# Kernel tuning notes

Measured on AMD Instinct MI355X. Metric: run time of the kernel, lower is better.

## Reference

```python
import jax, jax.numpy as jnp
import numpy as np

B, S, D = 8, 2048, 1024

def setup_inputs() -> dict:
    key = jax.random.key(0)
    ks = jax.random.split(key, 7)
    s = 1.0 / np.sqrt(D)
    return {
        "x": jax.random.normal(ks[0], (B, S, D), dtype=jnp.float32),
        "Wq": jax.random.normal(ks[1], (D, D), dtype=jnp.float32) * s,
        "bq": jnp.zeros((D,), dtype=jnp.float32),
        "Wk": jax.random.normal(ks[2], (D, D), dtype=jnp.float32) * s,
        "bk": jnp.zeros((D,), dtype=jnp.float32),
        "Wv": jax.random.normal(ks[3], (D, D), dtype=jnp.float32) * s,
        "bv": jnp.zeros((D,), dtype=jnp.float32),
    }

def reference(x, Wq, bq, Wk, bk, Wv, bv):
    # QKV projections: [B,S,D]
    q = x @ Wq + bq
    k = x @ Wk + bk
    v = x @ Wv + bv
    # scores scaled by sqrt(full input_dim) — single head, per source
    scores = jnp.einsum("bsd,btd->bst", q, k) / jnp.sqrt(jnp.float32(D))
    attn = jax.nn.softmax(scores, axis=2)
    return jnp.einsum("bst,btd->bsd", attn, v)
```

## Files before the change

### kernel.cpp

```cpp
#include <hip/hip_runtime.h>

typedef _Float16 half8 __attribute__((ext_vector_type(8)));
typedef float floatx4 __attribute__((ext_vector_type(4)));

#define AS1 __attribute__((address_space(1)))
#define AS3 __attribute__((address_space(3)))

__global__ __launch_bounds__(256) void wtrans_kernel(
    const float* __restrict__ W0, const float* __restrict__ W1,
    const float* __restrict__ W2, _Float16* __restrict__ Wt)
{
    __shared__ _Float16 t[64 * 72];
    const float* W = (blockIdx.z == 0) ? W0 : (blockIdx.z == 1) ? W1 : W2;
    _Float16* O = Wt + (long)blockIdx.z * 1048576;
    const int tid = threadIdx.x;
    const int kb = blockIdx.y * 64, nb = blockIdx.x * 64;
#pragma unroll
    for (int i = 0; i < 4; i++) {
        int r = (tid >> 4) + i * 16;
        int c = (tid & 15) * 4;
        floatx4 w = *(const floatx4*)&W[(long)(kb + r) * 1024 + nb + c];
#pragma unroll
        for (int j = 0; j < 4; j++) t[(c + j) * 72 + r] = (_Float16)w[j];
    }
    __syncthreads();
    const int c = tid >> 2, rch = (tid & 3) * 16;
    half8 v0 = *(const half8*)&t[c * 72 + rch];
    half8 v1 = *(const half8*)&t[c * 72 + rch + 8];
    _Float16* o = &O[(long)(nb + c) * 1024 + kb + rch];
    *(half8*)o = v0;
    *(half8*)(o + 8) = v1;
}

__global__ __launch_bounds__(256) void f32_to_f16_kernel(
    const float* __restrict__ in, _Float16* __restrict__ out, int n)
{
    for (long i = ((long)blockIdx.x * 256 + threadIdx.x) * 8; i < n;
         i += (long)gridDim.x * 256 * 8) {
        floatx4 a = *(const floatx4*)&in[i];
        floatx4 b = *(const floatx4*)&in[i + 4];
        half8 h;
#pragma unroll
        for (int e = 0; e < 4; e++) { h[e] = (_Float16)a[e]; h[e + 4] = (_Float16)b[e]; }
        *(half8*)&out[i] = h;
    }
}

template <int MODE>
__global__ __launch_bounds__(256) void gemm128_kernel(
    const _Float16* __restrict__ A, const _Float16* __restrict__ Bt,
    void* __restrict__ Cv, const float* __restrict__ bias,
    const float* __restrict__ bias2, float* __restrict__ R,
    int nx, int ny,
    int K, int lda, int ldb, int ldc,
    long aBatch, long bBatch, long cBatch, float scale)
{
    constexpr int SMEM_ELEMS = (MODE == 1) ? 17408 : 16384;
    __shared__ _Float16 smem[SMEM_ELEMS];
    _Float16* Ash = smem;
    _Float16* Bsh = smem + 8192;

    const int tid = threadIdx.x;
    const int wave = tid >> 6, lane = tid & 63;
    const int quad = lane >> 4, lr = lane & 15;
    const int wm = wave & 1, wn = wave >> 1;

    const int P = gridDim.x >> 3;
    const int g = (blockIdx.x & 7) * P + (blockIdx.x >> 3);
    const int pplane = nx * ny;
    const int z = g / pplane;
    const int rr = g - z * pplane;
    const int by = rr / nx;
    const int bx = rr - by * nx;
    const int m0 = by * 128, n0 = bx * 128;

    const _Float16* Ab = A + (long)z * aBatch;
    const _Float16* Bb = Bt + (long)z * bBatch;

    const int srow = tid >> 2;
    const int scol = ((tid & 3) ^ ((srow >> 1) & 3)) * 8;
    const long ag0 = (long)(m0 + srow) * lda + scol;
    const long bg0 = (long)(n0 + srow) * ldb + scol;
    const int sdst = tid * 8;

    floatx4 acc[4][4] = {};

    for (int k0 = 0; k0 < K; k0 += 64) {
#pragma unroll
        for (int s = 0; s < 2; s++) {
            const int kk = k0 + s * 32;
            const int so = s * 4096;
            __builtin_amdgcn_global_load_lds(
                (AS1 void*)(Ab + ag0 + kk), (AS3 void*)(Ash + so + sdst), 16, 0, 0);
            __builtin_amdgcn_global_load_lds(
                (AS1 void*)(Ab + ag0 + (long)64 * lda + kk), (AS3 void*)(Ash + so + sdst + 2048), 16, 0, 0);
            __builtin_amdgcn_global_load_lds(
                (AS1 void*)(Bb + bg0 + kk), (AS3 void*)(Bsh + so + sdst), 16, 0, 0);
            __builtin_amdgcn_global_load_lds(
                (AS1 void*)(Bb + bg0 + (long)64 * ldb + kk), (AS3 void*)(Bsh + so + sdst + 2048), 16, 0, 0);
        }
        __syncthreads();

        const int slotA = (quad ^ ((lr >> 1) & 3)) * 8;
#pragma unroll
        for (int s = 0; s < 2; s++) {
            const int so = s * 4096;
            half8 aF[4], bF[4];
#pragma unroll
            for (int i = 0; i < 4; i++) {
                aF[i] = *(const half8*)&Ash[so + (wm * 64 + i * 16 + lr) * 32 + slotA];
                bF[i] = *(const half8*)&Bsh[so + (wn * 64 + i * 16 + lr) * 32 + slotA];
            }
#pragma unroll
            for (int mi = 0; mi < 4; mi++)
#pragma unroll
                for (int ni = 0; ni < 4; ni++)
                    acc[mi][ni] = __builtin_amdgcn_mfma_f32_16x16x32_f16(
                        aF[mi], bF[ni], acc[mi][ni], 0, 0, 0);
        }
        __syncthreads();
    }

    if constexpr (MODE == 0) {
        _Float16* C = (_Float16*)Cv + (long)z * cBatch;
        const float* bz = (z == 0 || !bias2) ? bias : bias2;
#pragma unroll
        for (int ni = 0; ni < 4; ni++) {
            const int n = n0 + wn * 64 + ni * 16 + lr;
            const float bv_ = bz ? bz[n] : 0.0f;
#pragma unroll
            for (int mi = 0; mi < 4; mi++) {
                const int mb = m0 + wm * 64 + mi * 16 + quad * 4;
#pragma unroll
                for (int r = 0; r < 4; r++)
                    C[(long)(mb + r) * ldc + n] = (_Float16)(acc[mi][ni][r] + bv_);
            }
        }
    } else if constexpr (MODE == 1) {
        _Float16* ctile = smem;
#pragma unroll
        for (int ni = 0; ni < 4; ni++) {
            const int nl = wn * 64 + ni * 16 + lr;
            const float bv_ = bias ? bias[n0 + nl] : 0.0f;
#pragma unroll
            for (int mi = 0; mi < 4; mi++) {
                const int ml = wm * 64 + mi * 16 + quad * 4;
#pragma unroll
                for (int r = 0; r < 4; r++)
                    ctile[nl * 136 + ml + r] = (_Float16)(acc[mi][ni][r] + bv_);
            }
        }
        __syncthreads();
        _Float16* C = (_Float16*)Cv + (long)(m0 >> 11) * cBatch;
        const int t0 = m0 & 2047;
#pragma unroll
        for (int p = 0; p < 8; p++) {
            const int row = p * 16 + (tid >> 4);
            const int seg = (tid & 15) * 8;
            half8 v = *(const half8*)&ctile[row * 136 + seg];
            *(half8*)&C[(long)(n0 + row) * ldc + t0 + seg] = v;
        }
    } else if constexpr (MODE == 2) {
        float* C = (float*)Cv + (long)z * cBatch;
        const float* Rz = R + (long)z * 2048;
        float inv[4][4];
#pragma unroll
        for (int mi = 0; mi < 4; mi++) {
            const int mb = m0 + wm * 64 + mi * 16 + quad * 4;
#pragma unroll
            for (int r = 0; r < 4; r++) inv[mi][r] = 1.0f / Rz[mb + r];
        }
#pragma unroll
        for (int ni = 0; ni < 4; ni++) {
            const int n = n0 + wn * 64 + ni * 16 + lr;
#pragma unroll
            for (int mi = 0; mi < 4; mi++) {
                const int mb = m0 + wm * 64 + mi * 16 + quad * 4;
#pragma unroll
                for (int r = 0; r < 4; r++)
                    C[(long)(mb + r) * ldc + n] = acc[mi][ni][r] * inv[mi][r];
            }
        }
    } else {
        _Float16* C = (_Float16*)Cv + (long)z * cBatch;
        float* Rz = R + (long)z * 2048;
        float rs[4][4] = {};
#pragma unroll
        for (int ni = 0; ni < 4; ni++) {
            const int n = n0 + wn * 64 + ni * 16 + lr;
#pragma unroll
            for (int mi = 0; mi < 4; mi++) {
                const int mb = m0 + wm * 64 + mi * 16 + quad * 4;
#pragma unroll
                for (int r = 0; r < 4; r++) {
                    float e = __expf(acc[mi][ni][r] * scale);
                    C[(long)(mb + r) * ldc + n] = (_Float16)e;
                    rs[mi][r] += e;
                }
            }
        }
#pragma unroll
        for (int off = 1; off < 16; off <<= 1)
#pragma unroll
            for (int mi = 0; mi < 4; mi++)
#pragma unroll
                for (int r = 0; r < 4; r++)
                    rs[mi][r] += __shfl_xor(rs[mi][r], off, 64);
        if (lr == 0) {
#pragma unroll
            for (int mi = 0; mi < 4; mi++) {
                const int mb = m0 + wm * 64 + mi * 16 + quad * 4;
#pragma unroll
                for (int r = 0; r < 4; r++)
                    atomicAdd(&Rz[mb + r], rs[mi][r]);
            }
        }
    }
}

extern "C" void kernel_launch(void* const* d_in, const int* in_sizes, int n_in,
                              void* d_out, int out_size, void* d_ws, size_t ws_size,
                              hipStream_t stream)
{
    const float* x  = (const float*)d_in[0];
    const float* Wq = (const float*)d_in[1];
    const float* bq = (const float*)d_in[2];
    const float* Wk = (const float*)d_in[3];
    const float* bk = (const float*)d_in[4];
    const float* Wv = (const float*)d_in[5];
    const float* bv = (const float*)d_in[6];

    if (ws_size < 174129152u) return;

    char* ws = (char*)d_ws;
    _Float16* Q  = (_Float16*)(ws + 0);
    _Float16* Vt = (_Float16*)(ws + 67108864);
    _Float16* Sc = (_Float16*)(ws + 100663296);
    _Float16* Wt = (_Float16*)(ws + 167772160);
    float*    R  = (float*)(ws + 174063616);
    _Float16* xb = Sc;
    _Float16* Kb = Q + 16777216;
    float* out = (float*)d_out;

    hipMemsetAsync(R, 0, 65536, stream);
    wtrans_kernel<<<dim3(16, 16, 3), 256, 0, stream>>>(Wq, Wk, Wv, Wt);
    f32_to_f16_kernel<<<2048, 256, 0, stream>>>(x, xb, 16777216);

    gemm128_kernel<0><<<2048, 256, 0, stream>>>(
        xb, Wt, Q, bq, bk, nullptr, 8, 128, 1024, 1024, 1024, 1024,
        0, 1048576, 16777216, 1.0f);
    gemm128_kernel<1><<<1024, 256, 0, stream>>>(
        xb, Wt + 2097152, Vt, bv, nullptr, nullptr, 8, 128, 1024, 1024, 1024, 2048,
        0, 0, 2097152, 1.0f);

    gemm128_kernel<3><<<2048, 256, 0, stream>>>(
        Q, Kb, Sc, nullptr, nullptr, R, 16, 16, 1024, 1024, 1024, 2048,
        2097152, 2097152, 4194304, 0.03125f);

    gemm128_kernel<2><<<1024, 256, 0, stream>>>(
        Sc, Vt, out, nullptr, nullptr, R, 8, 16, 2048, 2048, 2048, 1024,
        4194304, 2097152, 2097152, 1.0f);
}
```

Before: 480.5 us.

## Add producer warp with triple-buffered LDS ring for GEMM loads

Each GEMM block gains a fifth wave that acts as a dedicated producer. It issues global-to-LDS loads into a three-stage ring buffer and signals the four consumer waves through shared-memory ready/done counters, replacing the two block-wide barriers per K step. The aim is to overlap memory loads with MFMA compute. It adds spin-waiting, more LDS per block (about 48KB, which may reduce occupancy) and a subtle synchronisation protocol. The softmax row-sum atomics are also reworked so each lane issues one atomic instead of lane 0 issuing sixteen.

```diff
diff --git a/kernel.cpp b/kernel.cpp
--- a/kernel.cpp
+++ b/kernel.cpp
@@ -5,6 +5,8 @@
 
 #define AS1 __attribute__((address_space(1)))
 #define AS3 __attribute__((address_space(3)))
+
+#define WAIT_VMCNT(n) __builtin_amdgcn_s_waitcnt(((n) & 15) | (((n) >> 4) << 14) | (7 << 4) | (15 << 8))
 
 __global__ __launch_bounds__(256) void wtrans_kernel(
     const float* __restrict__ W0, const float* __restrict__ W1,
@@ -47,7 +49,7 @@
 }
 
 template <int MODE>
-__global__ __launch_bounds__(256) void gemm128_kernel(
+__global__ __launch_bounds__(320) void gemm128_kernel(
     const _Float16* __restrict__ A, const _Float16* __restrict__ Bt,
     void* __restrict__ Cv, const float* __restrict__ bias,
     const float* __restrict__ bias2, float* __restrict__ R,
@@ -55,15 +57,13 @@
     int K, int lda, int ldb, int ldc,
     long aBatch, long bBatch, long cBatch, float scale)
 {
-    constexpr int SMEM_ELEMS = (MODE == 1) ? 17408 : 16384;
-    __shared__ _Float16 smem[SMEM_ELEMS];
-    _Float16* Ash = smem;
-    _Float16* Bsh = smem + 8192;
+    __shared__ _Float16 ring[3 * 8192];
+    __shared__ int ready;
+    __shared__ int done;
 
     const int tid = threadIdx.x;
-    const int wave = tid >> 6, lane = tid & 63;
-    const int quad = lane >> 4, lr = lane & 15;
-    const int wm = wave & 1, wn = wave >> 1;
+    if (tid == 0) { ready = 0; done = 0; }
+    __syncthreads();
 
     const int P = gridDim.x >> 3;
     const int g = (blockIdx.x & 7) * P + (blockIdx.x >> 3);
@@ -76,49 +76,81 @@
 
     const _Float16* Ab = A + (long)z * aBatch;
     const _Float16* Bb = Bt + (long)z * bBatch;
-
-    const int srow = tid >> 2;
-    const int scol = ((tid & 3) ^ ((srow >> 1) & 3)) * 8;
-    const long ag0 = (long)(m0 + srow) * lda + scol;
-    const long bg0 = (long)(n0 + srow) * ldb + scol;
-    const int sdst = tid * 8;
+    const int S = K >> 5;
+
+    if (tid >= 256) {
+        const int pl = tid - 256;
+        const int prow = pl >> 2;
+        const int pcol = (((pl & 3) ^ ((prow >> 1) & 3))) * 8;
+        const _Float16* aB = Ab + (long)(m0 + prow) * lda + pcol;
+        const _Float16* bB = Bb + (long)(n0 + prow) * ldb + pcol;
+
+        auto issue = [&](int s) {
+            _Float16* dst = ring + (s % 3) * 8192 + pl * 8;
+            const _Float16* a = aB + s * 32;
+            const _Float16* b = bB + s * 32;
+#pragma unroll
+            for (int i = 0; i < 8; i++)
+                __builtin_amdgcn_global_load_lds(
+                    (AS1 void*)(a + (long)i * 16 * lda), (AS3 void*)(dst + i * 512), 16, 0, 0);
+#pragma unroll
+            for (int i = 0; i < 8; i++)
+                __builtin_amdgcn_global_load_lds(
+                    (AS1 void*)(b + (long)i * 16 * ldb), (AS3 void*)(dst + 4096 + i * 512), 16, 0, 0);
+        };
+
+        issue(0);
+        issue(1);
+        int dn = 0;
+        for (int s = 0; s + 2 < S; s++) {
+            if (s >= 1 && dn < 4 * s) {
+                do {
+                    dn = __hip_atomic_load(&done, __ATOMIC_ACQUIRE, __HIP_MEMORY_SCOPE_WORKGROUP);
+                    if (dn < 4 * s) __builtin_amdgcn_s_sleep(1);
+                } while (dn < 4 * s);
+            }
+            issue(s + 2);
+            WAIT_VMCNT(32);
+            __hip_atomic_store(&ready, s + 1, __ATOMIC_RELEASE, __HIP_MEMORY_SCOPE_WORKGROUP);
+        }
+        WAIT_VMCNT(16);
+        __hip_atomic_store(&ready, S - 1, __ATOMIC_RELEASE, __HIP_MEMORY_SCOPE_WORKGROUP);
+        WAIT_VMCNT(0);
+        __hip_atomic_store(&ready, S, __ATOMIC_RELEASE, __HIP_MEMORY_SCOPE_WORKGROUP);
+        if constexpr (MODE == 1) { __syncthreads(); __syncthreads(); }
+        return;
+    }
+
+    const int wave = tid >> 6, lane = tid & 63;
+    const int quad = lane >> 4, lr = lane & 15;
+    const int wm = wave & 1, wn = wave >> 1;
+    const int slotA = (quad ^ ((lr >> 1) & 3)) * 8;
 
     floatx4 acc[4][4] = {};
-
-    for (int k0 = 0; k0 < K; k0 += 64) {
-#pragma unroll
-        for (int s = 0; s < 2; s++) {
-            const int kk = k0 + s * 32;
-            const int so = s * 4096;
-            __builtin_amdgcn_global_load_lds(
-                (AS1 void*)(Ab + ag0 + kk), (AS3 void*)(Ash + so + sdst), 16, 0, 0);
-            __builtin_amdgcn_global_load_lds(
-                (AS1 void*)(Ab + ag0 + (long)64 * lda + kk), (AS3 void*)(Ash + so + sdst + 2048), 16, 0, 0);
-            __builtin_amdgcn_global_load_lds(
-                (AS1 void*)(Bb + bg0 + kk), (AS3 void*)(Bsh + so + sdst), 16, 0, 0);
-            __builtin_amdgcn_global_load_lds(
-                (AS1 void*)(Bb + bg0 + (long)64 * ldb + kk), (AS3 void*)(Bsh + so + sdst + 2048), 16, 0, 0);
-        }
-        __syncthreads();
-
-        const int slotA = (quad ^ ((lr >> 1) & 3)) * 8;
-#pragma unroll
-        for (int s = 0; s < 2; s++) {
-            const int so = s * 4096;
-            half8 aF[4], bF[4];
-#pragma unroll
-            for (int i = 0; i < 4; i++) {
-                aF[i] = *(const half8*)&Ash[so + (wm * 64 + i * 16 + lr) * 32 + slotA];
-                bF[i] = *(const half8*)&Bsh[so + (wn * 64 + i * 16 + lr) * 32 + slotA];
-            }
-#pragma unroll
-            for (int mi = 0; mi < 4; mi++)
-#pragma unroll
-                for (int ni = 0; ni < 4; ni++)
-                    acc[mi][ni] = __builtin_amdgcn_mfma_f32_16x16x32_f16(
-                        aF[mi], bF[ni], acc[mi][ni], 0, 0, 0);
-        }
-        __syncthreads();
+    int rdy = 0;
+
+    for (int s = 0; s < S; s++) {
+        if (rdy < s + 1) {
+            do {
+                rdy = __hip_atomic_load(&ready, __ATOMIC_ACQUIRE, __HIP_MEMORY_SCOPE_WORKGROUP);
+            } while (rdy < s + 1);
+        }
+        const _Float16* As = ring + (s % 3) * 8192;
+        const _Float16* Bs = As + 4096;
+        half8 aF[4], bF[4];
+#pragma unroll
+        for (int i = 0; i < 4; i++) {
+            aF[i] = *(const half8*)&As[(wm * 64 + i * 16 + lr) * 32 + slotA];
+            bF[i] = *(const half8*)&Bs[(wn * 64 + i * 16 + lr) * 32 + slotA];
+        }
+#pragma unroll
+        for (int mi = 0; mi < 4; mi++)
+#pragma unroll
+            for (int ni = 0; ni < 4; ni++)
+                acc[mi][ni] = __builtin_amdgcn_mfma_f32_16x16x32_f16(
+                    aF[mi], bF[ni], acc[mi][ni], 0, 0, 0);
+        if (lane == 0)
+            __hip_atomic_fetch_add(&done, 1, __ATOMIC_RELEASE, __HIP_MEMORY_SCOPE_WORKGROUP);
     }
 
     if constexpr (MODE == 0) {
@@ -137,7 +169,8 @@
             }
         }
     } else if constexpr (MODE == 1) {
-        _Float16* ctile = smem;
+        __syncthreads();
+        _Float16* ctile = ring;
 #pragma unroll
         for (int ni = 0; ni < 4; ni++) {
             const int nl = wn * 64 + ni * 16 + lr;
@@ -206,15 +239,13 @@
 #pragma unroll
                 for (int r = 0; r < 4; r++)
                     rs[mi][r] += __shfl_xor(rs[mi][r], off, 64);
-        if (lr == 0) {
-#pragma unroll
-            for (int mi = 0; mi < 4; mi++) {
-                const int mb = m0 + wm * 64 + mi * 16 + quad * 4;
-#pragma unroll
-                for (int r = 0; r < 4; r++)
-                    atomicAdd(&Rz[mb + r], rs[mi][r]);
-            }
-        }
+        float myv = rs[0][0];
+#pragma unroll
+        for (int mi = 0; mi < 4; mi++)
+#pragma unroll
+            for (int r = 0; r < 4; r++)
+                if (lr == mi * 4 + r) myv = rs[mi][r];
+        atomicAdd(&Rz[m0 + wm * 64 + (lr >> 2) * 16 + quad * 4 + (lr & 3)], myv);
     }
 }
 
@@ -246,18 +277,18 @@
     wtrans_kernel<<<dim3(16, 16, 3), 256, 0, stream>>>(Wq, Wk, Wv, Wt);
     f32_to_f16_kernel<<<2048, 256, 0, stream>>>(x, xb, 16777216);
 
-    gemm128_kernel<0><<<2048, 256, 0, stream>>>(
+    gemm128_kernel<0><<<2048, 320, 0, stream>>>(
         xb, Wt, Q, bq, bk, nullptr, 8, 128, 1024, 1024, 1024, 1024,
         0, 1048576, 16777216, 1.0f);
-    gemm128_kernel<1><<<1024, 256, 0, stream>>>(
+    gemm128_kernel<1><<<1024, 320, 0, stream>>>(
         xb, Wt + 2097152, Vt, bv, nullptr, nullptr, 8, 128, 1024, 1024, 1024, 2048,
         0, 0, 2097152, 1.0f);
 
-    gemm128_kernel<3><<<2048, 256, 0, stream>>>(
+    gemm128_kernel<3><<<2048, 320, 0, stream>>>(
         Q, Kb, Sc, nullptr, nullptr, R, 16, 16, 1024, 1024, 1024, 2048,
         2097152, 2097152, 4194304, 0.03125f);
 
-    gemm128_kernel<2><<<1024, 256, 0, stream>>>(
+    gemm128_kernel<2><<<1024, 320, 0, stream>>>(
         Sc, Vt, out, nullptr, nullptr, R, 8, 16, 2048, 2048, 2048, 1024,
         4194304, 2097152, 2097152, 1.0f);
 }
```

New measurement: 666.6 us. 1.39x slower.
